# Kernel tuning notes

Measured on AMD Instinct MI355X. Metric: run time of the kernel, lower is better.

## Reference

```python
import jax, jax.numpy as jnp
import numpy as np

# Dimensions (match init_kwargs / input_specs)
B, C, H, W = 16, 16, 64, 64
N = H * W          # num_nodes
D_E = 64           # node_embed_dim
D_H = 128          # gnn_hidden_dim
D_R = 256          # readout_output_dim


def _param(key, shape, fan_in):
    return jax.random.normal(key, shape, jnp.float32) * (1.0 / np.sqrt(fan_in))


def setup_inputs() -> dict:
    key = jax.random.key(0)
    ks = jax.random.split(key, 16)
    inp = {
        "obs": jax.random.normal(ks[0], (B, C, H, W), jnp.float32),
        # node_embedding MLP (2 layers: C -> D_E -> D_E)
        "e1_w": _param(ks[1], (C, D_E), C),   "e1_b": jnp.zeros((D_E,), jnp.float32),
        "e2_w": _param(ks[2], (D_E, D_E), D_E), "e2_b": jnp.zeros((D_E,), jnp.float32),
        # 3 GNN layers (Linear then adjacency aggregation)
        "g1_w": _param(ks[3], (D_E, D_H), D_E), "g1_b": jnp.zeros((D_H,), jnp.float32),
        "g2_w": _param(ks[4], (D_H, D_H), D_H), "g2_b": jnp.zeros((D_H,), jnp.float32),
        "g3_w": _param(ks[5], (D_H, D_H), D_H), "g3_b": jnp.zeros((D_H,), jnp.float32),
        # readout MLP (2 layers: D_H -> 2*D_H -> D_R)
        "r1_w": _param(ks[6], (D_H, 2 * D_H), D_H),   "r1_b": jnp.zeros((2 * D_H,), jnp.float32),
        "r2_w": _param(ks[7], (2 * D_H, D_R), 2 * D_H), "r2_b": jnp.zeros((D_R,), jnp.float32),
    }
    return inp


def _adj_norm():
    # 4-neighbor grid adjacency on an H x W grid, row-normalized (same for every
    # batch element, so build once as (N, N) instead of (B, N, N)).
    idx = jnp.arange(N)
    up = jnp.eye(N, k=-W, dtype=jnp.float32)                      # i > 0
    down = jnp.eye(N, k=W, dtype=jnp.float32)                     # i < H-1
    left = jnp.eye(N, k=-1, dtype=jnp.float32) * ((idx % W) != 0)[:, None]
    right = jnp.eye(N, k=1, dtype=jnp.float32) * ((idx % W) != (W - 1))[:, None]
    adj = up + down + left + right
    return adj / (adj.sum(axis=1, keepdims=True) + 1e-6)


def reference(obs, e1_w, e1_b, e2_w, e2_b,
              g1_w, g1_b, g2_w, g2_b, g3_w, g3_b,
              r1_w, r1_b, r2_w, r2_b):
    relu = jax.nn.relu
    # grid -> graph: (B, C, H, W) -> (B, N, C)
    x = jnp.transpose(obs, (0, 2, 3, 1)).reshape(B, N, C)
    # node embedding MLP (output activation per ding MLP default)
    h = relu(x @ e1_w + e1_b)
    h = relu(h @ e2_w + e2_b)
    A = _adj_norm()  # (N, N)
    for Wg, bg in ((g1_w, g1_b), (g2_w, g2_b), (g3_w, g3_b)):
        support = h @ Wg + bg                      # (B, N, D_H)
        h = relu(jnp.einsum('nm,bmf->bnf', A, support))
    g = h.mean(axis=1)                              # (B, D_H) graph readout
    g = relu(g @ r1_w + r1_b)
    return relu(g @ r2_w + r2_b)                    # (B, D_R)
```

## Files before the change

kernel.cpp:

```cpp
#include <hip/hip_runtime.h>


typedef __attribute__((ext_vector_type(8))) short bf16x8;
typedef __attribute__((ext_vector_type(4))) float f32x4;
#define MFMA(a, b, c) __builtin_amdgcn_mfma_f32_16x16x32_bf16(a, b, c, 0, 0, 0)

__device__ inline void block_sync_lgkm() {
    asm volatile("" ::: "memory");
    __builtin_amdgcn_s_waitcnt(0xC07F);
    __builtin_amdgcn_s_barrier();
    asm volatile("" ::: "memory");
}

__device__ inline ushort bf16h(float x) {
    unsigned u = __float_as_uint(x);
    return (ushort)((u + 0x7fffu + ((u >> 16) & 1u)) >> 16);
}
__device__ inline void split_bf16(float x, ushort& hi, ushort& lo) {
    hi = bf16h(x);
    lo = bf16h(x - __uint_as_float(((unsigned)hi) << 16));
}
__device__ inline unsigned pack_split(float x) {
    unsigned u = __float_as_uint(x);
    unsigned hi = (u + 0x7fffu + ((u >> 16) & 1u)) >> 16;
    float r = x - __uint_as_float(hi << 16);
    return (hi << 16) | (__float_as_uint(r) >> 16);
}
__device__ inline void frag_packed(const unsigned* bp, bf16x8& bh, bf16x8& bl) {
    unsigned p[8];
#pragma unroll
    for (int j = 0; j < 8; j++) p[j] = bp[j * 65];
    union { bf16x8 v; unsigned d[4]; } H, L;
#pragma unroll
    for (int j = 0; j < 4; j++) {
        const unsigned e = p[2 * j], o = p[2 * j + 1];
        H.d[j] = (o & 0xFFFF0000u) | (e >> 16);
        L.d[j] = (o << 16) | (e & 0xFFFFu);
    }
    bh = H.v; bl = L.v;
}

__global__ __launch_bounds__(256, 4) void prep_embed_kernel(
    const float* __restrict__ obs,
    const float* __restrict__ e1w, const float* __restrict__ e1b,
    const float* __restrict__ e2w, const float* __restrict__ e2b,
    const float* __restrict__ g1w, const float* __restrict__ g2w,
    const float* __restrict__ g3w, ushort* __restrict__ wf,
    float* __restrict__ gsum, float* __restrict__ h0)
{
    const int blk = blockIdx.x, tid = threadIdx.x;

    if (blk < 20) {
        const int u = blk * 4 + (tid >> 6);
        const int l = tid & 63;
        const float* src; int K, kc, t; ushort* dst;
        if (u < 16)      { src = g1w; K = 64;  kc = u >> 3;        t = u & 7; dst = wf + 12288; }
        else if (u < 48) { src = g2w; K = 128; kc = (u - 16) >> 3; t = (u - 16) & 7; dst = wf + 28672; }
        else             { src = g3w; K = 128; kc = (u - 48) >> 3; t = (u - 48) & 7; dst = wf + 61440; }
        ushort* uh = dst + ((kc * 8 + t) * 2 + 0) * 512 + l * 8;
        ushort* ul = dst + ((kc * 8 + t) * 2 + 1) * 512 + l * 8;
        const int f = t * 16 + (l & 15);
        const int kb = kc * 32 + ((l >> 4) << 3);
#pragma unroll
        for (int j = 0; j < 8; j++) {
            const int k = kb + j;
            const float w = (k < K) ? src[k * 128 + f] : 0.f;
            ushort hi, lo; split_bf16(w, hi, lo);
            uh[j] = hi; ul[j] = lo;
        }
        return;
    }
    if (blk < 28) {
        gsum[(blk - 20) * 256 + tid] = 0.f;
        return;
    }

    __shared__ unsigned lds[6240];
    const int eb = blk - 28;
    const int ebid = ((eb & 7) << 7) | (eb >> 3);
    const int b = ebid >> 6, row = ebid & 63;
    const int lane = tid & 63, w = tid >> 6, quad = lane >> 4, nl = lane & 15;
    const int cp = tid >> 4, nq = tid & 15;

    const float4 x4 = *(const float4*)(obs + ((size_t)(b * 16 + cp) << 12) + row * 64 + nq * 4);

    {
        float* wr = (float*)lds;
#pragma unroll
        for (int i = 0; i < 20; i++) {
            const int idx = tid + 256 * i;
            wr[idx] = (idx < 1024) ? e1w[idx] : e2w[idx - 1024];
        }
    }
    __syncthreads();

    bf16x8 e1h, e1l, e2h[2], e2l[2];
    {
        const float* wr = (const float*)lds;
        const int f = 16 * w + nl;
#pragma unroll
        for (int j = 0; j < 8; j++) {
            const int k = quad * 8 + j;
            const float v = (k < 16) ? wr[k * 64 + f] : 0.f;
            ushort hi, lo; split_bf16(v, hi, lo);
            e1h[j] = (short)hi; e1l[j] = (short)lo;
        }
#pragma unroll
        for (int kc = 0; kc < 2; kc++)
#pragma unroll
            for (int j = 0; j < 8; j++) {
                const int k = kc * 32 + quad * 8 + j;
                const float v = wr[1024 + k * 64 + f];
                ushort hi, lo; split_bf16(v, hi, lo);
                e2h[kc][j] = (short)hi; e2l[kc][j] = (short)lo;
            }
    }
    __syncthreads();

    unsigned* Xs = lds;
    unsigned* Hs = lds + 2080;
    {
        unsigned* xp = Xs + cp * 65 + nq * 4;
        xp[0] = pack_split(x4.x); xp[1] = pack_split(x4.y);
        xp[2] = pack_split(x4.z); xp[3] = pack_split(x4.w);
        unsigned* zp = Xs + (16 + cp) * 65 + nq * 4;
        zp[0] = 0u; zp[1] = 0u; zp[2] = 0u; zp[3] = 0u;
    }
    __syncthreads();

#pragma unroll
    for (int nt = 0; nt < 4; nt++) {
        const unsigned* bp = Xs + (quad * 8) * 65 + nt * 16 + nl;
        bf16x8 bh, bl; frag_packed(bp, bh, bl);
        f32x4 c = {0.f, 0.f, 0.f, 0.f};
        c = MFMA(e1h, bh, c); c = MFMA(e1h, bl, c); c = MFMA(e1l, bh, c);
#pragma unroll
        for (int reg = 0; reg < 4; reg++) {
            const int fm = 16 * w + quad * 4 + reg;
            Hs[fm * 65 + nt * 16 + nl] = pack_split(fmaxf(c[reg] + e1b[fm], 0.f));
        }
    }
    __syncthreads();

    f32x4 a2[4];
#pragma unroll
    for (int nt = 0; nt < 4; nt++) a2[nt] = (f32x4){0.f, 0.f, 0.f, 0.f};
#pragma unroll
    for (int kc = 0; kc < 2; kc++) {
#pragma unroll
        for (int nt = 0; nt < 4; nt++) {
            const unsigned* bp = Hs + (kc * 32 + quad * 8) * 65 + nt * 16 + nl;
            bf16x8 bh, bl; frag_packed(bp, bh, bl);
            a2[nt] = MFMA(e2h[kc], bh, a2[nt]);
            a2[nt] = MFMA(e2h[kc], bl, a2[nt]);
            a2[nt] = MFMA(e2l[kc], bh, a2[nt]);
        }
    }
#pragma unroll
    for (int reg = 0; reg < 4; reg++) {
        const int f = 16 * w + quad * 4 + reg;
        const float bv = e2b[f];
#pragma unroll
        for (int nt = 0; nt < 4; nt++)
            h0[((size_t)(b * 64 + f) << 12) + row * 64 + nt * 16 + nl] =
                fmaxf(a2[nt][reg] + bv, 0.f);
    }
}

template <int K, bool MEAN>
__global__ __launch_bounds__(256, 4) void gnn_kernel(
    const float* __restrict__ hin, const ushort* __restrict__ wf,
    const float* __restrict__ bias, float* __restrict__ hout,
    float* __restrict__ gsum)
{
    constexpr int NQ = K / 32;
    __shared__ unsigned As[2][32 * 65];
    const int tid = threadIdx.x;
    const int bid = ((blockIdx.x & 7) << 7) | (blockIdx.x >> 3);
    const int b = bid >> 6, row = bid & 63;
    const int lane = tid & 63, w = tid >> 6, quad = lane >> 4, nl = lane & 15;
    const int kp = tid >> 4, nq = tid & 15;
    const float* hb = hin + (size_t)b * K * 4096;
    const int rowu = (row > 0) ? row - 1 : row;
    const int rowd = (row < 63) ? row + 1 : row;
    const float su = (row > 0) ? 1.f : 0.f;
    const float sd = (row < 63) ? 1.f : 0.f;
    float inv[4];
#pragma unroll
    for (int i = 0; i < 4; i++) {
        const int n = nq * 4 + i;
        const int deg = (row > 0) + (row < 63) + (n > 0) + (n < 63);
        inv[i] = 1.f / ((float)deg + 1e-6f);
    }

    const ushort* wfl = wf + lane * 8;
    f32x4 acc[4][2];
#pragma unroll
    for (int nt = 0; nt < 4; nt++) {
        acc[nt][0] = (f32x4){0.f, 0.f, 0.f, 0.f};
        acc[nt][1] = (f32x4){0.f, 0.f, 0.f, 0.f};
    }

    float4 S[6];
    bf16x8 V[2][2];

    auto sload = [&](int q) {
#pragma unroll
        for (int it = 0; it < 2; it++) {
            const int kg = q * 32 + it * 16 + kp;
            const float* pk = hb + ((size_t)kg << 12) + nq * 4;
            S[it * 3 + 0] = *(const float4*)(pk + row * 64);
            S[it * 3 + 1] = *(const float4*)(pk + rowu * 64);
            S[it * 3 + 2] = *(const float4*)(pk + rowd * 64);
        }
    };
    auto wload = [&](int q) {
#pragma unroll
        for (int ftl = 0; ftl < 2; ftl++) {
            V[ftl][0] = *(const bf16x8*)(wfl + ((q * 8 + 2 * w + ftl) * 2) * 512);
            V[ftl][1] = *(const bf16x8*)(wfl + ((q * 8 + 2 * w + ftl) * 2 + 1) * 512);
        }
    };
    auto stage = [&](unsigned* Ab) {
#pragma unroll
        for (int it = 0; it < 2; it++) {
            const int kl = it * 16 + kp;
            const float4 c4 = S[it * 3 + 0];
            const float4 u4 = S[it * 3 + 1];
            const float4 d4 = S[it * 3 + 2];
            const float pw = __shfl_up(c4.w, 1);
            const float nx = __shfl_down(c4.x, 1);
            const float lx = (nq > 0) ? pw : 0.f;
            const float rw = (nq < 15) ? nx : 0.f;
            unsigned* ap = Ab + kl * 65 + nq * 4;
            ap[0] = pack_split((su * u4.x + sd * d4.x + lx + c4.y) * inv[0]);
            ap[1] = pack_split((su * u4.y + sd * d4.y + c4.x + c4.z) * inv[1]);
            ap[2] = pack_split((su * u4.z + sd * d4.z + c4.y + c4.w) * inv[2]);
            ap[3] = pack_split((su * u4.w + sd * d4.w + c4.z + rw) * inv[3]);
        }
    };
    auto consume = [&](const unsigned* Ab) {
#pragma unroll
        for (int nt = 0; nt < 4; nt++) {
            const unsigned* bp = Ab + (quad * 8) * 65 + nt * 16 + nl;
            bf16x8 bh, bl; frag_packed(bp, bh, bl);
            acc[nt][0] = MFMA(V[0][0], bh, acc[nt][0]);
            acc[nt][0] = MFMA(V[0][0], bl, acc[nt][0]);
            acc[nt][0] = MFMA(V[0][1], bh, acc[nt][0]);
            acc[nt][1] = MFMA(V[1][0], bh, acc[nt][1]);
            acc[nt][1] = MFMA(V[1][0], bl, acc[nt][1]);
            acc[nt][1] = MFMA(V[1][1], bh, acc[nt][1]);
        }
    };

    wload(0);
    sload(0);
    stage(As[0]);
    sload(1);
    block_sync_lgkm();

#pragma unroll
    for (int q = 0; q < NQ; q++) {
        consume(As[q & 1]);
        if (q + 1 < NQ) {
            wload(q + 1);
            stage(As[(q + 1) & 1]);
            if (q + 2 < NQ) sload(q + 2);
            block_sync_lgkm();
        }
    }

    if (!MEAN) {
#pragma unroll
        for (int ftl = 0; ftl < 2; ftl++) {
            const int fb = 32 * w + 16 * ftl + quad * 4;
            const float b0 = bias[fb], b1 = bias[fb + 1], b2 = bias[fb + 2], b3 = bias[fb + 3];
#pragma unroll
            for (int nt = 0; nt < 4; nt++) {
                const int n = 16 * nt + nl;
                const int deg = (row > 0) + (row < 63) + (n > 0) + (n < 63);
                const float rs = (float)deg / ((float)deg + 1e-6f);
                float* op = hout + ((size_t)(b * 128 + fb) << 12) + row * 64 + n;
                op[0]        = fmaxf(acc[nt][ftl][0] + rs * b0, 0.f);
                op[1u << 12] = fmaxf(acc[nt][ftl][1] + rs * b1, 0.f);
                op[2u << 12] = fmaxf(acc[nt][ftl][2] + rs * b2, 0.f);
                op[3u << 12] = fmaxf(acc[nt][ftl][3] + rs * b3, 0.f);
            }
        }
    } else {
#pragma unroll
        for (int ftl = 0; ftl < 2; ftl++) {
            const int fb = 32 * w + 16 * ftl + quad * 4;
#pragma unroll
            for (int reg = 0; reg < 4; reg++) {
                const float bv = bias[fb + reg];
                float v = 0.f;
#pragma unroll
                for (int nt = 0; nt < 4; nt++) {
                    const int n = 16 * nt + nl;
                    const int deg = (row > 0) + (row < 63) + (n > 0) + (n < 63);
                    const float rs = (float)deg / ((float)deg + 1e-6f);
                    v += fmaxf(acc[nt][ftl][reg] + rs * bv, 0.f);
                }
                v += __shfl_xor(v, 1); v += __shfl_xor(v, 2);
                v += __shfl_xor(v, 4); v += __shfl_xor(v, 8);
                if (nl == 0) atomicAdd(&gsum[b * 128 + fb + reg], v * (1.f / 4096.f));
            }
        }
    }
}

__global__ __launch_bounds__(256) void readout_kernel(
    const float* __restrict__ gsum, const float* __restrict__ r1w,
    const float* __restrict__ r1b, const float* __restrict__ r2w,
    const float* __restrict__ r2b, float* __restrict__ out)
{
    __shared__ float gs[128];
    __shared__ float g2[256];
    const int b = blockIdx.x, tid = threadIdx.x;
    if (tid < 128) gs[tid] = gsum[b * 128 + tid];
    __syncthreads();
    float a = r1b[tid];
#pragma unroll 16
    for (int k = 0; k < 128; k++) a = fmaf(gs[k], r1w[k * 256 + tid], a);
    g2[tid] = fmaxf(a, 0.f);
    __syncthreads();
    float a2 = r2b[tid];
#pragma unroll 16
    for (int k = 0; k < 256; k++) a2 = fmaf(g2[k], r2w[k * 256 + tid], a2);
    out[b * 256 + tid] = fmaxf(a2, 0.f);
}

extern "C" void kernel_launch(void* const* d_in, const int* in_sizes, int n_in,
                              void* d_out, int out_size, void* d_ws, size_t ws_size,
                              hipStream_t stream)
{
    const float* obs = (const float*)d_in[0];
    const float* e1w = (const float*)d_in[1];
    const float* e1b = (const float*)d_in[2];
    const float* e2w = (const float*)d_in[3];
    const float* e2b = (const float*)d_in[4];
    const float* g1w = (const float*)d_in[5];
    const float* g1b = (const float*)d_in[6];
    const float* g2w = (const float*)d_in[7];
    const float* g2b = (const float*)d_in[8];
    const float* g3w = (const float*)d_in[9];
    const float* g3b = (const float*)d_in[10];
    const float* r1w = (const float*)d_in[11];
    const float* r1b = (const float*)d_in[12];
    const float* r2w = (const float*)d_in[13];
    const float* r2b = (const float*)d_in[14];
    float* out = (float*)d_out;
    float* ws = (float*)d_ws;

    float* h0 = ws;
    float* h1 = ws + 4194304;
    float* h2 = ws + 4194304 + 8388608;
    float* gsum = (float*)((char*)d_ws + 80u * 1024u * 1024u);
    ushort* wfb = (ushort*)((char*)d_ws + 80u * 1024u * 1024u + 8192u);

    hipLaunchKernelGGL(prep_embed_kernel, dim3(1052), dim3(256), 0, stream,
                       obs, e1w, e1b, e2w, e2b, g1w, g2w, g3w, wfb, gsum, h0);
    hipLaunchKernelGGL((gnn_kernel<64, false>), dim3(1024), dim3(256), 0, stream,
                       h0, wfb + 12288, g1b, h1, nullptr);
    hipLaunchKernelGGL((gnn_kernel<128, false>), dim3(1024), dim3(256), 0, stream,
                       h1, wfb + 28672, g2b, h2, nullptr);
    hipLaunchKernelGGL((gnn_kernel<128, true>), dim3(1024), dim3(256), 0, stream,
                       h2, wfb + 61440, g3b, nullptr, gsum);
    hipLaunchKernelGGL(readout_kernel, dim3(16), dim3(256), 0, stream,
                       gsum, r1w, r1b, r2w, r2b, out);
}
```

Measured before the change: 159.0 us.

## Fuse three GNN layers into one kernel with neighbor-row flag synchronization

Replaces the three separate GNN layer launches with a single kernel that runs all three layers in sequence. Between layers each block publishes a per-row ready flag and spins only on the flags of the rows directly above and below, instead of waiting at a full kernel boundary. Flags are zeroed by extra blocks in the prep kernel. This removes two launch gaps and the per-layer tail, but it depends on all 1024 blocks being resident at once. It also relies on relaxed atomics without an explicit release/acquire fence, so visibility of the neighbor data is a correctness risk, and the spin has a timeout escape.

```diff
diff --git a/kernel.cpp b/kernel.cpp
--- a/kernel.cpp
+++ b/kernel.cpp
@@ -46,7 +46,8 @@
     const float* __restrict__ e2w, const float* __restrict__ e2b,
     const float* __restrict__ g1w, const float* __restrict__ g2w,
     const float* __restrict__ g3w, ushort* __restrict__ wf,
-    float* __restrict__ gsum, float* __restrict__ h0)
+    float* __restrict__ gsum, float* __restrict__ h0,
+    unsigned* __restrict__ flags)
 {
     const int blk = blockIdx.x, tid = threadIdx.x;
 
@@ -74,9 +75,13 @@
         gsum[(blk - 20) * 256 + tid] = 0.f;
         return;
     }
+    if (blk < 36) {
+        flags[(blk - 28) * 256 + tid] = 0u;
+        return;
+    }
 
     __shared__ unsigned lds[6240];
-    const int eb = blk - 28;
+    const int eb = blk - 36;
     const int ebid = ((eb & 7) << 7) | (eb >> 3);
     const int b = ebid >> 6, row = ebid & 63;
     const int lane = tid & 63, w = tid >> 6, quad = lane >> 4, nl = lane & 15;
@@ -167,31 +172,35 @@
     }
 }
 
+__device__ inline void spin_flag(const unsigned* p) {
+    int n = 0;
+    while (__hip_atomic_load(p, __ATOMIC_RELAXED, __HIP_MEMORY_SCOPE_AGENT) == 0u) {
+        __builtin_amdgcn_s_sleep(2);
+        if (++n > (1 << 24)) break;
+    }
+}
+__device__ inline void wait_nb(const unsigned* fl, int bid, int row, int tid) {
+    if (tid == 0  && row > 0)  spin_flag(fl + bid - 1);
+    if (tid == 64 && row < 63) spin_flag(fl + bid + 1);
+    __syncthreads();
+    asm volatile("" ::: "memory");
+}
+
 template <int K, bool MEAN>
-__global__ __launch_bounds__(256, 4) void gnn_kernel(
-    const float* __restrict__ hin, const ushort* __restrict__ wf,
-    const float* __restrict__ bias, float* __restrict__ hout,
-    float* __restrict__ gsum)
+__device__ __forceinline__ void gnn_layer(
+    const float* __restrict__ hb,
+    const ushort* __restrict__ wf, const float* __restrict__ bias,
+    float* __restrict__ houtb,
+    float* __restrict__ gsum, int b,
+    unsigned* AsB, int row, int tid, const float* inv)
 {
     constexpr int NQ = K / 32;
-    __shared__ unsigned As[2][32 * 65];
-    const int tid = threadIdx.x;
-    const int bid = ((blockIdx.x & 7) << 7) | (blockIdx.x >> 3);
-    const int b = bid >> 6, row = bid & 63;
     const int lane = tid & 63, w = tid >> 6, quad = lane >> 4, nl = lane & 15;
     const int kp = tid >> 4, nq = tid & 15;
-    const float* hb = hin + (size_t)b * K * 4096;
     const int rowu = (row > 0) ? row - 1 : row;
     const int rowd = (row < 63) ? row + 1 : row;
     const float su = (row > 0) ? 1.f : 0.f;
     const float sd = (row < 63) ? 1.f : 0.f;
-    float inv[4];
-#pragma unroll
-    for (int i = 0; i < 4; i++) {
-        const int n = nq * 4 + i;
-        const int deg = (row > 0) + (row < 63) + (n > 0) + (n < 63);
-        inv[i] = 1.f / ((float)deg + 1e-6f);
-    }
 
     const ushort* wfl = wf + lane * 8;
     f32x4 acc[4][2];
@@ -255,16 +264,16 @@
 
     wload(0);
     sload(0);
-    stage(As[0]);
+    stage(AsB);
     sload(1);
     block_sync_lgkm();
 
 #pragma unroll
     for (int q = 0; q < NQ; q++) {
-        consume(As[q & 1]);
+        consume(AsB + (q & 1) * 2080);
         if (q + 1 < NQ) {
             wload(q + 1);
-            stage(As[(q + 1) & 1]);
+            stage(AsB + ((q + 1) & 1) * 2080);
             if (q + 2 < NQ) sload(q + 2);
             block_sync_lgkm();
         }
@@ -280,7 +289,7 @@
                 const int n = 16 * nt + nl;
                 const int deg = (row > 0) + (row < 63) + (n > 0) + (n < 63);
                 const float rs = (float)deg / ((float)deg + 1e-6f);
-                float* op = hout + ((size_t)(b * 128 + fb) << 12) + row * 64 + n;
+                float* op = houtb + ((size_t)fb << 12) + row * 64 + n;
                 op[0]        = fmaxf(acc[nt][ftl][0] + rs * b0, 0.f);
                 op[1u << 12] = fmaxf(acc[nt][ftl][1] + rs * b1, 0.f);
                 op[2u << 12] = fmaxf(acc[nt][ftl][2] + rs * b2, 0.f);
@@ -308,6 +317,44 @@
             }
         }
     }
+}
+
+__global__ __launch_bounds__(256, 4) void gnn_fused_kernel(
+    const float* __restrict__ h0, float* __restrict__ h1,
+    float* __restrict__ h2, const ushort* __restrict__ wfb,
+    const float* __restrict__ g1b, const float* __restrict__ g2b,
+    const float* __restrict__ g3b, float* __restrict__ gsum,
+    unsigned* __restrict__ flags)
+{
+    __shared__ unsigned As[2 * 2080];
+    const int tid = threadIdx.x;
+    const int bid = ((blockIdx.x & 7) << 7) | (blockIdx.x >> 3);
+    const int b = bid >> 6, row = bid & 63;
+    const int nq = tid & 15;
+    float inv[4];
+#pragma unroll
+    for (int i = 0; i < 4; i++) {
+        const int n = nq * 4 + i;
+        const int deg = (row > 0) + (row < 63) + (n > 0) + (n < 63);
+        inv[i] = 1.f / ((float)deg + 1e-6f);
+    }
+
+    gnn_layer<64, false>(h0 + (size_t)b * 64 * 4096, wfb + 12288, g1b,
+                         h1 + (size_t)b * 128 * 4096, nullptr, b, As, row, tid, inv);
+    __syncthreads();
+    if (tid == 0)
+        __hip_atomic_store(flags + bid, 1u, __ATOMIC_RELAXED, __HIP_MEMORY_SCOPE_AGENT);
+    wait_nb(flags, bid, row, tid);
+
+    gnn_layer<128, false>(h1 + (size_t)b * 128 * 4096, wfb + 28672, g2b,
+                          h2 + (size_t)b * 128 * 4096, nullptr, b, As, row, tid, inv);
+    __syncthreads();
+    if (tid == 0)
+        __hip_atomic_store(flags + 1024 + bid, 1u, __ATOMIC_RELAXED, __HIP_MEMORY_SCOPE_AGENT);
+    wait_nb(flags + 1024, bid, row, tid);
+
+    gnn_layer<128, true>(h2 + (size_t)b * 128 * 4096, wfb + 61440, g3b,
+                         nullptr, gsum, b, As, row, tid, inv);
 }
 
 __global__ __launch_bounds__(256) void readout_kernel(
@@ -358,15 +405,12 @@
     float* h2 = ws + 4194304 + 8388608;
     float* gsum = (float*)((char*)d_ws + 80u * 1024u * 1024u);
     ushort* wfb = (ushort*)((char*)d_ws + 80u * 1024u * 1024u + 8192u);
-
-    hipLaunchKernelGGL(prep_embed_kernel, dim3(1052), dim3(256), 0, stream,
-                       obs, e1w, e1b, e2w, e2b, g1w, g2w, g3w, wfb, gsum, h0);
-    hipLaunchKernelGGL((gnn_kernel<64, false>), dim3(1024), dim3(256), 0, stream,
-                       h0, wfb + 12288, g1b, h1, nullptr);
-    hipLaunchKernelGGL((gnn_kernel<128, false>), dim3(1024), dim3(256), 0, stream,
-                       h1, wfb + 28672, g2b, h2, nullptr);
-    hipLaunchKernelGGL((gnn_kernel<128, true>), dim3(1024), dim3(256), 0, stream,
-                       h2, wfb + 61440, g3b, nullptr, gsum);
+    unsigned* flags = (unsigned*)((char*)d_ws + 80u * 1024u * 1024u + 8192u + 196608u);
+
+    hipLaunchKernelGGL(prep_embed_kernel, dim3(1060), dim3(256), 0, stream,
+                       obs, e1w, e1b, e2w, e2b, g1w, g2w, g3w, wfb, gsum, h0, flags);
+    hipLaunchKernelGGL(gnn_fused_kernel, dim3(1024), dim3(256), 0, stream,
+                       h0, h1, h2, wfb, g1b, g2b, g3b, gsum, flags);
     hipLaunchKernelGGL(readout_kernel, dim3(16), dim3(256), 0, stream,
                        gsum, r1w, r1b, r2w, r2b, out);
 }
```

Result: slower. 183.6 us (+15.4%).
